# Kernel tuning notes

Measured on AMD Instinct MI355X. Metric: run time of the kernel, lower is better.

The kernel has to match this reference:

```python
import jax, jax.numpy as jnp
import numpy as np

NEG_SLOPE = 0.01  # torch.nn.LeakyReLU default


def setup_inputs() -> dict:
    key = jax.random.key(0)
    ks = jax.random.split(key, 9)
    N_W, N_I, E = 100000, 100000, 2000000
    C_IN, C_OUT, N_CLS = 256, 64, 10
    sc_in = 1.0 / np.sqrt(C_IN)
    sc_cat = 1.0 / np.sqrt(2 * C_OUT)
    return {
        "x_worker": jax.random.normal(ks[0], (N_W, C_IN), dtype=jnp.float32),
        "x_item": jax.random.normal(ks[1], (N_I, C_IN), dtype=jnp.float32),
        "edge_index": jax.random.randint(ks[2], (2, E), 0, N_W, dtype=jnp.int32),
        "W_worker": jax.random.uniform(ks[3], (C_IN, C_OUT), jnp.float32, -sc_in, sc_in),
        "b_worker": jax.random.uniform(ks[4], (C_OUT,), jnp.float32, -sc_in, sc_in),
        "W_item": jax.random.uniform(ks[5], (C_IN, C_OUT), jnp.float32, -sc_in, sc_in),
        "b_item": jax.random.uniform(ks[6], (C_OUT,), jnp.float32, -sc_in, sc_in),
        "W_edge": jax.random.uniform(ks[7], (2 * C_OUT, N_CLS), jnp.float32, -sc_cat, sc_cat),
        "b_edge": jax.random.uniform(ks[8], (N_CLS,), jnp.float32, -sc_cat, sc_cat),
    }


def reference(x_worker, x_item, edge_index, W_worker, b_worker, W_item, b_item, W_edge, b_edge):
    # encoders: Linear + LeakyReLU  -> [N, C_OUT]
    xw = jax.nn.leaky_relu(x_worker @ W_worker + b_worker, NEG_SLOPE)
    xi = jax.nn.leaky_relu(x_item @ W_item + b_item, NEG_SLOPE)
    # gather endpoints per edge and concat -> [E, 2*C_OUT]
    x_cat = jnp.concatenate([xw[edge_index[0]], xi[edge_index[1]]], axis=-1)
    logits = x_cat @ W_edge + b_edge  # [E, num_class]
    return xw, xi, jax.nn.log_softmax(logits, axis=-1)
```

## Files before the change

kernel.cpp:

```cpp
#include <hip/hip_runtime.h>
#include <hip/hip_bf16.h>

#define LOG2E 1.4426950408889634f
#define LN2   0.6931471805599453f

typedef __attribute__((ext_vector_type(8))) short bf16x8;
typedef __attribute__((ext_vector_type(4))) float f32x4;

static __device__ __forceinline__ short f2bf(float f) {
  __hip_bfloat16 h = __float2bfloat16(f);
  return *reinterpret_cast<short*>(&h);
}

static __device__ __forceinline__ void gll16(const float* gsrc, float* ldst) {
  __builtin_amdgcn_global_load_lds(
      (const __attribute__((address_space(1))) void*)gsrc,
      (__attribute__((address_space(3))) void*)ldst, 16, 0, 0);
}

__global__ __launch_bounds__(256) void wprep_kernel(
    const float* __restrict__ Ww, const float* __restrict__ Wi,
    ushort* __restrict__ wfrag)
{
  int id = blockIdx.x * 256 + threadIdx.x;
  if (id >= 4096) return;
  int enc  = id >> 11;
  int f    = (id >> 6) & 31;
  int l    = id & 63;
  int nsub = f >> 3, ks = f & 7;
  const float* __restrict__ W = enc ? Wi : Ww;
  int n  = nsub * 16 + (l & 15);
  int k0 = ks * 32 + (l >> 4) * 8;
  ushort* dst = wfrag + ((size_t)(enc * 32 + f) * 64 + l) * 8;
#pragma unroll
  for (int j = 0; j < 8; ++j)
    dst[j] = (ushort)f2bf(W[(size_t)(k0 + j) * 64 + n]);
}

__global__ __launch_bounds__(256, 1) void enc_mfma3_kernel(
    const float* __restrict__ x0, const float* __restrict__ b0,
    const float* __restrict__ x1, const float* __restrict__ b1,
    const ushort* __restrict__ wfrag, float* __restrict__ out, int M)
{
  __shared__ ushort sfrag[16384];
  __shared__ float  xstg[4][4096];

  const int enc = blockIdx.y;
  const float* __restrict__ x   = enc ? x1 : x0;
  const float* __restrict__ bia = enc ? b1 : b0;
  float* __restrict__ o = out + (size_t)enc * (size_t)M * 64u;

  const int lane = threadIdx.x & 63;
  const int wid  = threadIdx.x >> 6;
  const int rsel = lane & 15;
  const int kgrp = lane >> 4;
  const int swz  = rsel & 7;

  const int nstrips = (M + 15) >> 4;
  int strip = blockIdx.x * 4 + wid;
  const int nw = gridDim.x * 4;

  float bv[4];
#pragma unroll
  for (int nsub = 0; nsub < 4; ++nsub) bv[nsub] = bia[nsub * 16 + rsel];

  {
    const f32x4* src = (const f32x4*)wfrag + (size_t)enc * 2048;
    f32x4* dst = (f32x4*)sfrag;
#pragma unroll
    for (int i = 0; i < 8; ++i)
      dst[threadIdx.x + 256 * i] = src[threadIdx.x + 256 * i];
  }
  __syncthreads();

  float* xw = xstg[wid];
  bool active = strip < nstrips;

  if (active) {
#pragma unroll
    for (int r = 0; r < 16; ++r) {
      int rg = strip * 16 + r; if (rg >= M) rg = M - 1;
      const float* gs = x + (size_t)rg * 256u + ((lane ^ (r & 7)) << 2);
      gll16(gs, xw + r * 256);
    }
  }

  while (active) {
    int next = strip + nw;

    asm volatile("s_waitcnt vmcnt(0)" ::: "memory");
    __builtin_amdgcn_sched_barrier(0);

    bf16x8 a[8];
#pragma unroll
    for (int ks = 0; ks < 8; ++ks) {
      int c0 = kgrp * 2 + ks * 8;
      f32x4 lo = *(const f32x4*)&xw[rsel * 256 + (((c0    ) ^ swz) << 2)];
      f32x4 hi = *(const f32x4*)&xw[rsel * 256 + (((c0 + 1) ^ swz) << 2)];
      a[ks][0] = f2bf(lo.x); a[ks][1] = f2bf(lo.y);
      a[ks][2] = f2bf(lo.z); a[ks][3] = f2bf(lo.w);
      a[ks][4] = f2bf(hi.x); a[ks][5] = f2bf(hi.y);
      a[ks][6] = f2bf(hi.z); a[ks][7] = f2bf(hi.w);
    }

    asm volatile("s_waitcnt lgkmcnt(0)" ::: "memory");
    __builtin_amdgcn_sched_barrier(0);

    if (next < nstrips) {
#pragma unroll
      for (int r = 0; r < 16; ++r) {
        int rg = next * 16 + r; if (rg >= M) rg = M - 1;
        const float* gs = x + (size_t)rg * 256u + ((lane ^ (r & 7)) << 2);
        gll16(gs, xw + r * 256);
      }
    }

    f32x4 acc[4];
#pragma unroll
    for (int nsub = 0; nsub < 4; ++nsub) acc[nsub] = f32x4{0.f, 0.f, 0.f, 0.f};
#pragma unroll
    for (int ks = 0; ks < 8; ++ks) {
#pragma unroll
      for (int nsub = 0; nsub < 4; ++nsub) {
        bf16x8 bfr = *(const bf16x8*)(sfrag + ((size_t)((nsub * 8 + ks) * 64 + lane)) * 8);
        acc[nsub] = __builtin_amdgcn_mfma_f32_16x16x32_bf16(a[ks], bfr, acc[nsub], 0, 0, 0);
      }
    }

    int crow = strip * 16 + kgrp * 4;
#pragma unroll
    for (int nsub = 0; nsub < 4; ++nsub) {
#pragma unroll
      for (int r = 0; r < 4; ++r) {
        int rr = crow + r;
        if (rr < M) {
          float v = acc[nsub][r] + bv[nsub];
          v = fmaxf(v, 0.01f * v);
          o[(size_t)rr * 64u + nsub * 16 + rsel] = v;
        }
      }
    }

    strip = next;
    active = next < nstrips;
  }
}

__global__ __launch_bounds__(256) void proj_kernel(
    const float* __restrict__ feats, const float* __restrict__ W_edge,
    float* __restrict__ ws, int M)
{
  const int enc = blockIdx.y;
  int row = blockIdx.x * 256 + threadIdx.x;
  if (row >= M) return;
  const float4* __restrict__ f4 =
      (const float4*)(feats + ((size_t)enc * M + row) * 64u);
  const float* __restrict__ W2 = W_edge + enc * 640;

  float acc[10];
#pragma unroll
  for (int k = 0; k < 10; ++k) acc[k] = 0.f;

#pragma unroll 4
  for (int n4 = 0; n4 < 16; ++n4) {
    float4 xv = f4[n4];
    const float* w = W2 + n4 * 40;
#pragma unroll
    for (int k = 0; k < 10; ++k) acc[k] = fmaf(xv.x, w[k],      acc[k]);
#pragma unroll
    for (int k = 0; k < 10; ++k) acc[k] = fmaf(xv.y, w[10 + k], acc[k]);
#pragma unroll
    for (int k = 0; k < 10; ++k) acc[k] = fmaf(xv.z, w[20 + k], acc[k]);
#pragma unroll
    for (int k = 0; k < 10; ++k) acc[k] = fmaf(xv.w, w[30 + k], acc[k]);
  }

  float* orow = ws + ((size_t)enc * M + row) * 16u;
#pragma unroll
  for (int k = 0; k < 10; ++k) orow[k] = acc[k];
  orow[10] = 0.f; orow[11] = 0.f;
}

__global__ __launch_bounds__(256) void edge_kernel(
    const int* __restrict__ ei, const float* __restrict__ ws,
    const float* __restrict__ b_edge, float* __restrict__ out,
    int E, int M)
{
  __shared__ float sm[256 * 11];
  long e = (long)blockIdx.x * 256 + threadIdx.x;
  float l[10];
#pragma unroll
  for (int k = 0; k < 10; ++k) l[k] = 0.f;

  if (e < E) {
    int e0 = ei[e];
    int e1 = ei[E + e];
    const float4* pw = (const float4*)ws + (size_t)e0 * 4u;
    const float4* pi = (const float4*)ws + ((size_t)M + e1) * 4u;
    float4 a0 = pw[0], a1 = pw[1], a2 = pw[2];
    float4 c0 = pi[0], c1 = pi[1], c2 = pi[2];
    l[0] = a0.x + c0.x + b_edge[0];
    l[1] = a0.y + c0.y + b_edge[1];
    l[2] = a0.z + c0.z + b_edge[2];
    l[3] = a0.w + c0.w + b_edge[3];
    l[4] = a1.x + c1.x + b_edge[4];
    l[5] = a1.y + c1.y + b_edge[5];
    l[6] = a1.z + c1.z + b_edge[6];
    l[7] = a1.w + c1.w + b_edge[7];
    l[8] = a2.x + c2.x + b_edge[8];
    l[9] = a2.y + c2.y + b_edge[9];
    float m = l[0];
#pragma unroll
    for (int k = 1; k < 10; ++k) m = fmaxf(m, l[k]);
    float s = 0.f;
#pragma unroll
    for (int k = 0; k < 10; ++k) { l[k] = (l[k] - m) * LOG2E; s += exp2f(l[k]); }
    float ls = log2f(s);
#pragma unroll
    for (int k = 0; k < 10; ++k) l[k] = (l[k] - ls) * LN2;
  }

#pragma unroll
  for (int k = 0; k < 10; ++k) sm[threadIdx.x * 11 + k] = l[k];
  __syncthreads();
  long obase = (long)blockIdx.x * 2560;
  long lim = (long)E * 10;
#pragma unroll
  for (int j = 0; j < 10; ++j) {
    int jj = j * 256 + threadIdx.x;
    long oi = obase + jj;
    if (oi < lim) out[oi] = sm[(jj / 10) * 11 + (jj % 10)];
  }
}

__global__ __launch_bounds__(256) void enc_kernel_f32(
    const float* __restrict__ x0, const float* __restrict__ W0, const float* __restrict__ b0,
    const float* __restrict__ x1, const float* __restrict__ W1, const float* __restrict__ b1,
    float* __restrict__ out, int M)
{
  const int enc = blockIdx.y;
  const float* __restrict__ x = enc ? x1 : x0;
  const float* __restrict__ W = enc ? W1 : W0;
  const float* __restrict__ b = enc ? b1 : b0;
  float* __restrict__ o = out + (size_t)enc * (size_t)M * 64u;

  const int lane = threadIdx.x & 63;
  const int wid  = threadIdx.x >> 6;
  int row0 = __builtin_amdgcn_readfirstlane(blockIdx.x * 64 + wid * 16);
  const float* __restrict__ xrow = x + (size_t)row0 * 256u;

  float acc[16];
#pragma unroll
  for (int r = 0; r < 16; ++r) acc[r] = 0.f;

  if (row0 + 16 <= M) {
#pragma unroll 4
    for (int k = 0; k < 256; ++k) {
      float wv = W[k * 64 + lane];
#pragma unroll
      for (int r = 0; r < 16; ++r)
        acc[r] = fmaf(xrow[r * 256 + k], wv, acc[r]);
    }
    float bias = b[lane];
#pragma unroll
    for (int r = 0; r < 16; ++r) {
      float v = acc[r] + bias;
      v = fmaxf(v, 0.01f * v);
      o[(size_t)(row0 + r) * 64u + lane] = v;
    }
  } else if (row0 < M) {
    int nr = M - row0;
    for (int k = 0; k < 256; ++k) {
      float wv = W[k * 64 + lane];
      for (int r = 0; r < nr; ++r)
        acc[r] = fmaf(xrow[r * 256 + k], wv, acc[r]);
    }
    float bias = b[lane];
    for (int r = 0; r < nr; ++r) {
      float v = acc[r] + bias;
      v = fmaxf(v, 0.01f * v);
      o[(size_t)(row0 + r) * 64u + lane] = v;
    }
  }
}

__global__ __launch_bounds__(256) void edge_kernel_direct(
    const int* __restrict__ ei, const float* __restrict__ feats,
    const float* __restrict__ W_edge, const float* __restrict__ b_edge,
    float* __restrict__ out, int E, int M)
{
  __shared__ float sm[256 * 11];
  long e = (long)blockIdx.x * 256 + threadIdx.x;
  float l[10];
#pragma unroll
  for (int k = 0; k < 10; ++k) l[k] = 0.f;

  if (e < E) {
    int e0 = ei[e];
    int e1 = ei[E + e];
#pragma unroll
    for (int k = 0; k < 10; ++k) l[k] = b_edge[k];
    const float4* fw = (const float4*)(feats + (size_t)e0 * 64u);
    const float4* fi = (const float4*)(feats + ((size_t)M + e1) * 64u);
#pragma unroll 4
    for (int n4 = 0; n4 < 16; ++n4) {
      float4 xv = fw[n4];
      const float* w = W_edge + n4 * 40;
#pragma unroll
      for (int k = 0; k < 10; ++k) l[k] = fmaf(xv.x, w[k],      l[k]);
#pragma unroll
      for (int k = 0; k < 10; ++k) l[k] = fmaf(xv.y, w[10 + k], l[k]);
#pragma unroll
      for (int k = 0; k < 10; ++k) l[k] = fmaf(xv.z, w[20 + k], l[k]);
#pragma unroll
      for (int k = 0; k < 10; ++k) l[k] = fmaf(xv.w, w[30 + k], l[k]);
    }
#pragma unroll 4
    for (int n4 = 0; n4 < 16; ++n4) {
      float4 xv = fi[n4];
      const float* w = W_edge + 640 + n4 * 40;
#pragma unroll
      for (int k = 0; k < 10; ++k) l[k] = fmaf(xv.x, w[k],      l[k]);
#pragma unroll
      for (int k = 0; k < 10; ++k) l[k] = fmaf(xv.y, w[10 + k], l[k]);
#pragma unroll
      for (int k = 0; k < 10; ++k) l[k] = fmaf(xv.z, w[20 + k], l[k]);
#pragma unroll
      for (int k = 0; k < 10; ++k) l[k] = fmaf(xv.w, w[30 + k], l[k]);
    }
    float m = l[0];
#pragma unroll
    for (int k = 1; k < 10; ++k) m = fmaxf(m, l[k]);
    float s = 0.f;
#pragma unroll
    for (int k = 0; k < 10; ++k) { l[k] = (l[k] - m) * LOG2E; s += exp2f(l[k]); }
    float ls = log2f(s);
#pragma unroll
    for (int k = 0; k < 10; ++k) l[k] = (l[k] - ls) * LN2;
  }

#pragma unroll
  for (int k = 0; k < 10; ++k) sm[threadIdx.x * 11 + k] = l[k];
  __syncthreads();
  long obase = (long)blockIdx.x * 2560;
  long lim = (long)E * 10;
#pragma unroll
  for (int j = 0; j < 10; ++j) {
    int jj = j * 256 + threadIdx.x;
    long oi = obase + jj;
    if (oi < lim) out[oi] = sm[(jj / 10) * 11 + (jj % 10)];
  }
}

extern "C" void kernel_launch(void* const* d_in, const int* in_sizes, int n_in,
                              void* d_out, int out_size, void* d_ws, size_t ws_size,
                              hipStream_t stream)
{
  const float* x_w = (const float*)d_in[0];
  const float* x_i = (const float*)d_in[1];
  const int*   ei  = (const int*)d_in[2];
  const float* W_w = (const float*)d_in[3];
  const float* b_w = (const float*)d_in[4];
  const float* W_i = (const float*)d_in[5];
  const float* b_i = (const float*)d_in[6];
  const float* W_e = (const float*)d_in[7];
  const float* b_e = (const float*)d_in[8];
  float* out = (float*)d_out;

  const int M = in_sizes[0] / 256;
  const int E = in_sizes[2] / 2;

  float* logout = out + (size_t)2 * (size_t)M * 64u;

  const size_t pw_bytes = (size_t)2 * (size_t)M * 16u * sizeof(float);
  const size_t ws_need  = pw_bytes + 65536;

  if (ws_size >= ws_need) {
    float*  ws    = (float*)d_ws;
    ushort* wfrag = (ushort*)((char*)d_ws + pw_bytes);

    wprep_kernel<<<16, 256, 0, stream>>>(W_w, W_i, wfrag);

    dim3 gA(128, 2);
    enc_mfma3_kernel<<<gA, 256, 0, stream>>>(x_w, b_w, x_i, b_i, wfrag, out, M);

    dim3 gB((M + 255) / 256, 2);
    proj_kernel<<<gB, 256, 0, stream>>>(out, W_e, ws, M);

    dim3 gC((unsigned)((E + 255) / 256));
    edge_kernel<<<gC, 256, 0, stream>>>(ei, ws, b_e, logout, E, M);
  } else {
    dim3 gA0((M + 63) / 64, 2);
    enc_kernel_f32<<<gA0, 256, 0, stream>>>(x_w, W_w, b_w, x_i, W_i, b_i, out, M);
    dim3 gC((unsigned)((E + 255) / 256));
    edge_kernel_direct<<<gC, 256, 0, stream>>>(ei, out, W_e, b_e, logout, E, M);
  }
}
```

Measured before the change: 141.8 us.

## Restructure encoder to share row strips across warps with double-buffered staging

The MFMA encoder now has all four warps of a block work on the same 16-row strip, each computing one 16-column slice. Input rows go through a two-slot LDS double buffer with block barriers and vmcnt-based waits, replacing one private staging buffer per warp. Grid size and occupancy hint are doubled. The edge bias is folded into the worker projection, and the edge kernel's output copy is vectorised with an unpadded LDS layout; these aim to cut LDS use, raise occupancy and overlap loads, at the cost of extra block barriers and possible LDS bank conflicts.

Measured after the change: 142.4 us. Within noise of the previous version (+0.5%).

```diff
diff --git a/kernel.cpp b/kernel.cpp
--- a/kernel.cpp
+++ b/kernel.cpp
@@ -37,13 +37,13 @@
     dst[j] = (ushort)f2bf(W[(size_t)(k0 + j) * 64 + n]);
 }
 
-__global__ __launch_bounds__(256, 1) void enc_mfma3_kernel(
+__global__ __launch_bounds__(256, 2) void enc_mfma4_kernel(
     const float* __restrict__ x0, const float* __restrict__ b0,
     const float* __restrict__ x1, const float* __restrict__ b1,
     const ushort* __restrict__ wfrag, float* __restrict__ out, int M)
 {
   __shared__ ushort sfrag[16384];
-  __shared__ float  xstg[4][4096];
+  __shared__ float  xbuf[2][4096];
 
   const int enc = blockIdx.y;
   const float* __restrict__ x   = enc ? x1 : x0;
@@ -54,15 +54,10 @@
   const int wid  = threadIdx.x >> 6;
   const int rsel = lane & 15;
   const int kgrp = lane >> 4;
-  const int swz  = rsel & 7;
+  const int sw   = rsel & 7;
 
   const int nstrips = (M + 15) >> 4;
-  int strip = blockIdx.x * 4 + wid;
-  const int nw = gridDim.x * 4;
-
-  float bv[4];
-#pragma unroll
-  for (int nsub = 0; nsub < 4; ++nsub) bv[nsub] = bia[nsub * 16 + rsel];
+  const int bx = blockIdx.x, G = gridDim.x;
 
   {
     const f32x4* src = (const f32x4*)wfrag + (size_t)enc * 2048;
@@ -73,30 +68,48 @@
   }
   __syncthreads();
 
-  float* xw = xstg[wid];
-  bool active = strip < nstrips;
-
-  if (active) {
-#pragma unroll
-    for (int r = 0; r < 16; ++r) {
-      int rg = strip * 16 + r; if (rg >= M) rg = M - 1;
-      const float* gs = x + (size_t)rg * 256u + ((lane ^ (r & 7)) << 2);
-      gll16(gs, xw + r * 256);
-    }
-  }
-
-  while (active) {
-    int next = strip + nw;
-
+  const int niter = (bx < nstrips) ? ((nstrips - 1 - bx) / G + 1) : 0;
+  if (niter == 0) return;
+
+  const float bv = bia[wid * 16 + rsel];
+
+  auto stage = [&](int s, int buf) {
+#pragma unroll
+    for (int j = 0; j < 4; ++j) {
+      int R = wid * 4 + j;
+      int rg = s * 16 + R; if (rg >= M) rg = M - 1;
+      const float* gs = x + (size_t)rg * 256u + ((lane ^ (R & 7)) << 2);
+      gll16(gs, &xbuf[buf][R * 256]);
+    }
+  };
+
+  stage(bx, 0);
+  if (niter > 1) {
+    stage(bx + G, 1);
+    asm volatile("s_waitcnt vmcnt(4)" ::: "memory");
+  } else {
     asm volatile("s_waitcnt vmcnt(0)" ::: "memory");
+  }
+  __builtin_amdgcn_sched_barrier(0);
+
+  for (int i = 0; i < niter; ++i) {
+    const int s = bx + i * G;
+    if (i) {
+      if (i == niter - 1) asm volatile("s_waitcnt vmcnt(4)" ::: "memory");
+      else                asm volatile("s_waitcnt vmcnt(8)" ::: "memory");
+      __builtin_amdgcn_sched_barrier(0);
+    }
+    __builtin_amdgcn_s_barrier();
     __builtin_amdgcn_sched_barrier(0);
 
+    const float* xb = xbuf[i & 1];
+
     bf16x8 a[8];
 #pragma unroll
     for (int ks = 0; ks < 8; ++ks) {
-      int c0 = kgrp * 2 + ks * 8;
-      f32x4 lo = *(const f32x4*)&xw[rsel * 256 + (((c0    ) ^ swz) << 2)];
-      f32x4 hi = *(const f32x4*)&xw[rsel * 256 + (((c0 + 1) ^ swz) << 2)];
+      int c0 = ks * 8 + kgrp * 2;
+      f32x4 lo = *(const f32x4*)&xb[rsel * 256 + (((c0    ) ^ sw) << 2)];
+      f32x4 hi = *(const f32x4*)&xb[rsel * 256 + (((c0 + 1) ^ sw) << 2)];
       a[ks][0] = f2bf(lo.x); a[ks][1] = f2bf(lo.y);
       a[ks][2] = f2bf(lo.z); a[ks][3] = f2bf(lo.w);
       a[ks][4] = f2bf(hi.x); a[ks][5] = f2bf(hi.y);
@@ -105,50 +118,34 @@
 
     asm volatile("s_waitcnt lgkmcnt(0)" ::: "memory");
     __builtin_amdgcn_sched_barrier(0);
-
-    if (next < nstrips) {
-#pragma unroll
-      for (int r = 0; r < 16; ++r) {
-        int rg = next * 16 + r; if (rg >= M) rg = M - 1;
-        const float* gs = x + (size_t)rg * 256u + ((lane ^ (r & 7)) << 2);
-        gll16(gs, xw + r * 256);
+    __builtin_amdgcn_s_barrier();
+    __builtin_amdgcn_sched_barrier(0);
+
+    if (i + 2 < niter) stage(bx + (i + 2) * G, i & 1);
+
+    f32x4 acc = f32x4{0.f, 0.f, 0.f, 0.f};
+#pragma unroll
+    for (int ks = 0; ks < 8; ++ks) {
+      bf16x8 bfr = *(const bf16x8*)(sfrag + ((size_t)((wid * 8 + ks) * 64 + lane)) * 8);
+      acc = __builtin_amdgcn_mfma_f32_16x16x32_bf16(a[ks], bfr, acc, 0, 0, 0);
+    }
+
+    const int crow = s * 16 + kgrp * 4;
+#pragma unroll
+    for (int r = 0; r < 4; ++r) {
+      int rr = crow + r;
+      if (rr < M) {
+        float v = acc[r] + bv;
+        v = fmaxf(v, 0.01f * v);
+        o[(size_t)rr * 64u + wid * 16 + rsel] = v;
       }
     }
-
-    f32x4 acc[4];
-#pragma unroll
-    for (int nsub = 0; nsub < 4; ++nsub) acc[nsub] = f32x4{0.f, 0.f, 0.f, 0.f};
-#pragma unroll
-    for (int ks = 0; ks < 8; ++ks) {
-#pragma unroll
-      for (int nsub = 0; nsub < 4; ++nsub) {
-        bf16x8 bfr = *(const bf16x8*)(sfrag + ((size_t)((nsub * 8 + ks) * 64 + lane)) * 8);
-        acc[nsub] = __builtin_amdgcn_mfma_f32_16x16x32_bf16(a[ks], bfr, acc[nsub], 0, 0, 0);
-      }
-    }
-
-    int crow = strip * 16 + kgrp * 4;
-#pragma unroll
-    for (int nsub = 0; nsub < 4; ++nsub) {
-#pragma unroll
-      for (int r = 0; r < 4; ++r) {
-        int rr = crow + r;
-        if (rr < M) {
-          float v = acc[nsub][r] + bv[nsub];
-          v = fmaxf(v, 0.01f * v);
-          o[(size_t)rr * 64u + nsub * 16 + rsel] = v;
-        }
-      }
-    }
-
-    strip = next;
-    active = next < nstrips;
   }
 }
 
 __global__ __launch_bounds__(256) void proj_kernel(
     const float* __restrict__ feats, const float* __restrict__ W_edge,
-    float* __restrict__ ws, int M)
+    const float* __restrict__ b_edge, float* __restrict__ ws, int M)
 {
   const int enc = blockIdx.y;
   int row = blockIdx.x * 256 + threadIdx.x;
@@ -159,7 +156,7 @@
 
   float acc[10];
 #pragma unroll
-  for (int k = 0; k < 10; ++k) acc[k] = 0.f;
+  for (int k = 0; k < 10; ++k) acc[k] = enc ? 0.f : b_edge[k];
 
 #pragma unroll 4
   for (int n4 = 0; n4 < 16; ++n4) {
@@ -178,15 +175,13 @@
   float* orow = ws + ((size_t)enc * M + row) * 16u;
 #pragma unroll
   for (int k = 0; k < 10; ++k) orow[k] = acc[k];
-  orow[10] = 0.f; orow[11] = 0.f;
 }
 
 __global__ __launch_bounds__(256) void edge_kernel(
     const int* __restrict__ ei, const float* __restrict__ ws,
-    const float* __restrict__ b_edge, float* __restrict__ out,
-    int E, int M)
-{
-  __shared__ float sm[256 * 11];
+    float* __restrict__ out, int E, int M)
+{
+  __shared__ float sm[2560];
   long e = (long)blockIdx.x * 256 + threadIdx.x;
   float l[10];
 #pragma unroll
@@ -199,16 +194,9 @@
     const float4* pi = (const float4*)ws + ((size_t)M + e1) * 4u;
     float4 a0 = pw[0], a1 = pw[1], a2 = pw[2];
     float4 c0 = pi[0], c1 = pi[1], c2 = pi[2];
-    l[0] = a0.x + c0.x + b_edge[0];
-    l[1] = a0.y + c0.y + b_edge[1];
-    l[2] = a0.z + c0.z + b_edge[2];
-    l[3] = a0.w + c0.w + b_edge[3];
-    l[4] = a1.x + c1.x + b_edge[4];
-    l[5] = a1.y + c1.y + b_edge[5];
-    l[6] = a1.z + c1.z + b_edge[6];
-    l[7] = a1.w + c1.w + b_edge[7];
-    l[8] = a2.x + c2.x + b_edge[8];
-    l[9] = a2.y + c2.y + b_edge[9];
+    l[0] = a0.x + c0.x; l[1] = a0.y + c0.y; l[2] = a0.z + c0.z; l[3] = a0.w + c0.w;
+    l[4] = a1.x + c1.x; l[5] = a1.y + c1.y; l[6] = a1.z + c1.z; l[7] = a1.w + c1.w;
+    l[8] = a2.x + c2.x; l[9] = a2.y + c2.y;
     float m = l[0];
 #pragma unroll
     for (int k = 1; k < 10; ++k) m = fmaxf(m, l[k]);
@@ -221,15 +209,16 @@
   }
 
 #pragma unroll
-  for (int k = 0; k < 10; ++k) sm[threadIdx.x * 11 + k] = l[k];
+  for (int k = 0; k < 10; ++k) sm[threadIdx.x * 10 + k] = l[k];
   __syncthreads();
-  long obase = (long)blockIdx.x * 2560;
-  long lim = (long)E * 10;
-#pragma unroll
-  for (int j = 0; j < 10; ++j) {
-    int jj = j * 256 + threadIdx.x;
-    long oi = obase + jj;
-    if (oi < lim) out[oi] = sm[(jj / 10) * 11 + (jj % 10)];
+  const f32x4* sm4 = (const f32x4*)sm;
+  f32x4* ob = (f32x4*)(out + (size_t)blockIdx.x * 2560u);
+  long lim4 = ((long)E * 10) >> 2;
+  long base4 = (long)blockIdx.x * 640;
+#pragma unroll
+  for (int j = 0; j < 3; ++j) {
+    int idx = j * 256 + threadIdx.x;
+    if (idx < 640 && base4 + idx < lim4) ob[idx] = sm4[idx];
   }
 }
 
@@ -289,7 +278,7 @@
     const float* __restrict__ W_edge, const float* __restrict__ b_edge,
     float* __restrict__ out, int E, int M)
 {
-  __shared__ float sm[256 * 11];
+  __shared__ float sm[2560];
   long e = (long)blockIdx.x * 256 + threadIdx.x;
   float l[10];
 #pragma unroll
@@ -340,15 +329,16 @@
   }
 
 #pragma unroll
-  for (int k = 0; k < 10; ++k) sm[threadIdx.x * 11 + k] = l[k];
+  for (int k = 0; k < 10; ++k) sm[threadIdx.x * 10 + k] = l[k];
   __syncthreads();
-  long obase = (long)blockIdx.x * 2560;
-  long lim = (long)E * 10;
-#pragma unroll
-  for (int j = 0; j < 10; ++j) {
-    int jj = j * 256 + threadIdx.x;
-    long oi = obase + jj;
-    if (oi < lim) out[oi] = sm[(jj / 10) * 11 + (jj % 10)];
+  const f32x4* sm4 = (const f32x4*)sm;
+  f32x4* ob = (f32x4*)(out + (size_t)blockIdx.x * 2560u);
+  long lim4 = ((long)E * 10) >> 2;
+  long base4 = (long)blockIdx.x * 640;
+#pragma unroll
+  for (int j = 0; j < 3; ++j) {
+    int idx = j * 256 + threadIdx.x;
+    if (idx < 640 && base4 + idx < lim4) ob[idx] = sm4[idx];
   }
 }
 
@@ -381,14 +371,14 @@
 
     wprep_kernel<<<16, 256, 0, stream>>>(W_w, W_i, wfrag);
 
-    dim3 gA(128, 2);
-    enc_mfma3_kernel<<<gA, 256, 0, stream>>>(x_w, b_w, x_i, b_i, wfrag, out, M);
+    dim3 gA(256, 2);
+    enc_mfma4_kernel<<<gA, 256, 0, stream>>>(x_w, b_w, x_i, b_i, wfrag, out, M);
 
     dim3 gB((M + 255) / 256, 2);
-    proj_kernel<<<gB, 256, 0, stream>>>(out, W_e, ws, M);
+    proj_kernel<<<gB, 256, 0, stream>>>(out, W_e, b_e, ws, M);
 
     dim3 gC((unsigned)((E + 255) / 256));
-    edge_kernel<<<gC, 256, 0, stream>>>(ei, ws, b_e, logout, E, M);
+    edge_kernel<<<gC, 256, 0, stream>>>(ei, ws, logout, E, M);
   } else {
     dim3 gA0((M + 63) / 64, 2);
     enc_kernel_f32<<<gA0, 256, 0, stream>>>(x_w, W_w, b_w, x_i, W_i, b_i, out, M);
```
